# Kernel optimization log

Measured on AMD Instinct MI355X. Metric: run time of the kernel, lower is better.

The kernel has to match this reference:

```python
import jax, jax.numpy as jnp
import numpy as np

B, CI, HI, WI = 64, 3, 96, 96
G = 8
HG, WG = 16, 16
HIDLIN = 512
SIGMA_BOOST = 2.0
EPS = 1e-7
HID = (HI // 4 // 2) * (WI // 4 // 2) * 128  # 12*12*128 = 18432


def _conv(x, w, b):
    # NCHW conv, 3x3, padding 1 (matches nn.Conv2d(kernel_size=3, padding=1))
    y = jax.lax.conv_general_dilated(x, w, (1, 1), ((1, 1), (1, 1)),
                                     dimension_numbers=('NCHW', 'OIHW', 'NCHW'))
    return y + b[None, :, None, None]


def _maxpool(x, k):
    return jax.lax.reduce_window(x, -jnp.inf, jax.lax.max,
                                 (1, 1, k, k), (1, 1, k, k), 'VALID')


def setup_inputs() -> dict:
    key = jax.random.key(0)
    ks = jax.random.split(key, 22)

    def w(k, shape, fan_in):
        return jax.random.normal(k, shape, jnp.float32) * np.float32(1.0 / np.sqrt(fan_in))

    return {
        'image': jax.random.normal(ks[0], (B, CI, HI, WI), jnp.float32),
        'noise': jax.random.normal(ks[1], (B * G, 2), jnp.float32),
        # conv block 1
        'w1a': w(ks[2], (32, CI, 3, 3), CI * 9), 'b1a': jnp.zeros((32,), jnp.float32),
        'w1b': w(ks[3], (32, 32, 3, 3), 32 * 9), 'b1b': jnp.zeros((32,), jnp.float32),
        # conv block 2
        'w2a': w(ks[4], (64, 32, 3, 3), 32 * 9), 'b2a': jnp.zeros((64,), jnp.float32),
        'w2b': w(ks[5], (64, 64, 3, 3), 64 * 9), 'b2b': jnp.zeros((64,), jnp.float32),
        # conv block 3
        'w3a': w(ks[6], (128, 64, 3, 3), 64 * 9), 'b3a': jnp.zeros((128,), jnp.float32),
        'w3b': w(ks[7], (128, 128, 3, 3), 128 * 9), 'b3b': jnp.zeros((128,), jnp.float32),
        # linear head (weights stored (in, out))
        'wl1': w(ks[8], (HID, HIDLIN), HID), 'bl1': jnp.zeros((HIDLIN,), jnp.float32),
        'wl2': w(ks[9], (HIDLIN, HIDLIN), HIDLIN), 'bl2': jnp.zeros((HIDLIN,), jnp.float32),
        'wl3': w(ks[10], (HIDLIN, G * 3), HIDLIN), 'bl3': jnp.zeros((G * 3,), jnp.float32),
    }


def reference(image, noise, w1a, b1a, w1b, b1b, w2a, b2a, w2b, b2b,
              w3a, b3a, w3b, b3b, wl1, bl1, wl2, bl2, wl3, bl3):
    # --- preprocess CNN ---
    x = jax.nn.relu(_conv(image, w1a, b1a))
    x = jax.nn.relu(_conv(x, w1b, b1b))
    x = _maxpool(x, 4)
    x = jax.nn.relu(_conv(x, w2a, b2a))
    x = jax.nn.relu(_conv(x, w2b, b2b))
    x = _maxpool(x, 2)
    x = jax.nn.relu(_conv(x, w3a, b3a))
    x = jax.nn.relu(_conv(x, w3b, b3b))
    x = x.reshape(B, -1)                      # Flatten (C,H,W order, like torch .view)
    x = jax.nn.relu(x @ wl1 + bl1)
    x = jax.nn.relu(x @ wl2 + bl2)            # Linear(HIDLIN,HIDLIN) then the extra ReLU
    prep = (x @ wl3 + bl3).reshape(B * G, 3)  # (b*g, 3)

    means = prep[:, :2]                        # (b*g, 2) raw means
    sraw = prep[:, 2]
    # sparse.transform_sigmas: softplus(s + SIGMA_BOOST) + eps, scaled per spatial dim
    sig = jax.nn.softplus(sraw + SIGMA_BOOST) + EPS
    sigmas = sig[:, None] * jnp.array([HI - 1, WI - 1], jnp.float32)  # (b*g, 2)

    # Normal(means, sigmas).sample() -> reparameterized but detached (torch .sample())
    sample = jax.lax.stop_gradient(means + sigmas * noise)
    # sparse.transform_means over size (hi-hg, wi-wg): sigmoid * (size-1), then round
    msize = jnp.array([HI - HG - 1, WI - WG - 1], jnp.float32)
    pts = jnp.round(jax.nn.sigmoid(sample) * msize).astype(jnp.int32).reshape(B, G, 2)

    # glimpse extraction: the original's b*g python slicing loop -> vmapped dynamic_slice
    src = jax.lax.stop_gradient(image)  # original slices image.data (no grad)

    def ext_one(img, p):
        return jax.lax.dynamic_slice(img, (jnp.int32(0), p[0], p[1]), (CI, HG, WG))

    result = jax.vmap(lambda img, ps: jax.vmap(lambda p: ext_one(img, p))(ps))(src, pts)
    # result: (B, G, CI, HG, WG)
    return result, means.reshape(B, G, 2), sigmas.reshape(B, G, 2)
```

## Files before the change

kernel.cpp:

```cpp
#include <hip/hip_runtime.h>
#include <math.h>

constexpr int BB  = 64;
constexpr int CIc = 3;
constexpr int HIc = 96, WIc = 96;
constexpr int Gc  = 8, HGc = 16, WGc = 16;
constexpr int HIDc = 18432;
constexpr int HIDLINc = 512;

using short8 = __attribute__((ext_vector_type(8))) short;
using s4     = __attribute__((ext_vector_type(4))) short;
using f32x16 = __attribute__((ext_vector_type(16))) float;

__device__ inline unsigned short bfr(float f) {
    unsigned int u = __float_as_uint(f);
    u = (u + 0x7FFFu + ((u >> 16) & 1u)) >> 16;
    return (unsigned short)u;
}
__device__ inline float ubf(unsigned short s) {
    return __uint_as_float(((unsigned int)s) << 16);
}

__device__ __attribute__((aligned(16))) unsigned short g_wh[9216];
__device__ __attribute__((aligned(16))) unsigned short g_wm[9216];
__device__ __attribute__((aligned(16))) unsigned short g_wl[9216];

__device__ __attribute__((aligned(16))) unsigned short g_wph[276480];
__device__ __attribute__((aligned(16))) unsigned short g_wpm[276480];
__device__ __attribute__((aligned(16))) unsigned short g_wpl[276480];

__device__ inline void packN_one(const float* __restrict__ w, int CIN, int ofs,
                                 int idx)
{
    int chsz = 288 * CIN;
    int chunk = idx / chsz;
    int t = idx - chunk * chsz;
    int s = t >> 9;
    int rr = t & 511;
    int g = rr >> 8, oc32 = (rr >> 3) & 31, j = rr & 7;
    int nc16 = CIN / 16;
    int tap = s / nc16, c16 = s % nc16;
    int ci = c16 * 16 + g * 8 + j;
    int oc = chunk * 32 + oc32;
    float v = w[((size_t)oc * CIN + ci) * 9 + tap];
    unsigned short h = bfr(v);
    float r1 = v - ubf(h);
    unsigned short m = bfr(r1);
    g_wph[ofs + idx] = h; g_wpm[ofs + idx] = m; g_wpl[ofs + idx] = bfr(r1 - ubf(m));
}

__global__ void pack_all(const float* __restrict__ w1b, const float* __restrict__ w2a,
                         const float* __restrict__ w2b, const float* __restrict__ w3a,
                         const float* __restrict__ w3b)
{
    int idx = blockIdx.x * 256 + threadIdx.x;
    if (idx < 9216) {
        int j = idx & 7, oc = (idx >> 3) & 31, g = (idx >> 8) & 1, s = idx >> 9;
        int ci = 16 * (s & 1) + 8 * g + j;
        int tap = s >> 1;
        float v = w1b[(oc * 32 + ci) * 9 + tap];
        unsigned short h = bfr(v);
        float r1 = v - ubf(h);
        unsigned short m = bfr(r1);
        g_wh[idx] = h; g_wm[idx] = m; g_wl[idx] = bfr(r1 - ubf(m));
    } else if (idx < 27648) {
        packN_one(w2a, 32, 0, idx - 9216);
    } else if (idx < 64512) {
        packN_one(w2b, 64, 18432, idx - 27648);
    } else if (idx < 138240) {
        packN_one(w3a, 64, 55296, idx - 64512);
    } else if (idx < 285696) {
        packN_one(w3b, 128, 129024, idx - 138240);
    }
}

__device__ inline void bz_one(unsigned short* __restrict__ Xh,
                              unsigned short* __restrict__ Xm,
                              unsigned short* __restrict__ Xl,
                              int PAD, int C, int idx)
{
    int RING = 4 * PAD - 4;
    int ci = idx % C;
    int cell = (idx / C) % RING;
    int b = idx / (C * RING);
    int y, x;
    if (cell < PAD)          { y = 0;       x = cell; }
    else if (cell < 2 * PAD) { y = PAD - 1; x = cell - PAD; }
    else { int t = cell - 2 * PAD; y = 1 + (t >> 1); x = (t & 1) ? PAD - 1 : 0; }
    size_t a = ((size_t)(b * PAD + y) * PAD + x) * C + ci;
    Xh[a] = 0; Xm[a] = 0; Xl[a] = 0;
}

__global__ void border_all(unsigned short* X2h, unsigned short* X2m, unsigned short* X2l,
                           unsigned short* X3h, unsigned short* X3m, unsigned short* X3l,
                           unsigned short* X4h, unsigned short* X4m, unsigned short* X4l,
                           unsigned short* X5h, unsigned short* X5m, unsigned short* X5l)
{
    int idx = blockIdx.x * 256 + threadIdx.x;
    if (idx < 204800)        bz_one(X2h, X2m, X2l, 26, 32, idx);
    else if (idx < 614400)   bz_one(X3h, X3m, X3l, 26, 64, idx - 204800);
    else if (idx < 827392)   bz_one(X4h, X4m, X4l, 14, 64, idx - 614400);
    else if (idx < 1253376)  bz_one(X5h, X5m, X5l, 14, 128, idx - 827392);
}

__global__ __launch_bounds__(256)
void conv1ab(const float* __restrict__ image, const float* __restrict__ w1a,
             const float* __restrict__ b1a, const float* __restrict__ b1b,
             unsigned short* __restrict__ X2h, unsigned short* __restrict__ X2m,
             unsigned short* __restrict__ X2l)
{
    const int id    = blockIdx.x;
    const int xcd   = id & 7;
    const int local = id >> 3;
    const int gblk  = xcd * 576 + local;
    const int b  = gblk / 72;
    const int r  = gblk % 72;
    const int yq = r / 3;
    const int xt = r % 3;

    const int tid = threadIdx.x;
    const int wave = tid >> 6, lane = tid & 63;
    const int col = lane & 31, g = lane >> 5;

    __shared__ float s_img[3][8][36];
    __shared__ __align__(16) short s_hml[3][6][34][36];
    __shared__ float s_pool[4][8][2][16];
    __shared__ float s_b1b[32];
    if (tid < 32) s_b1b[tid] = b1b[tid];

    for (int idx = tid; idx < 3 * 8 * 36; idx += 256) {
        int ci = idx / 288;
        int rem = idx - ci * 288;
        int rr = rem / 36, cc = rem - rr * 36;
        int gy = 4 * yq - 2 + rr, gx = 32 * xt - 2 + cc;
        float v = 0.0f;
        if (gy >= 0 && gy < 96 && gx >= 0 && gx < 96)
            v = image[((size_t)(b * 3 + ci) * 96 + gy) * 96 + gx];
        s_img[ci][rr][cc] = v;
    }
    __syncthreads();

    if (tid < 204) {
        int lr = tid / 34, lc = tid - (tid / 34) * 34;
        int gr = 4 * yq - 1 + lr, gc = 32 * xt - 1 + lc;
        bool valid = (gr >= 0 && gr < 96 && gc >= 0 && gc < 96);
        float acc[32];
#pragma unroll
        for (int oc = 0; oc < 32; ++oc) acc[oc] = 0.0f;
        if (valid) {
#pragma unroll
            for (int ci = 0; ci < 3; ++ci) {
                float v[3][3];
#pragma unroll
                for (int dy = 0; dy < 3; ++dy)
#pragma unroll
                    for (int dx = 0; dx < 3; ++dx)
                        v[dy][dx] = s_img[ci][lr + dy][lc + dx];
#pragma unroll
                for (int oc = 0; oc < 32; ++oc) {
                    const float* w9 = w1a + ((size_t)oc * 3 + ci) * 9;
                    float a = acc[oc];
#pragma unroll
                    for (int dy = 0; dy < 3; ++dy)
#pragma unroll
                        for (int dx = 0; dx < 3; ++dx)
                            a = fmaf(v[dy][dx], w9[dy * 3 + dx], a);
                    acc[oc] = a;
                }
            }
        }
#pragma unroll
        for (int q = 0; q < 8; ++q) {
            s4 H, M, L;
#pragma unroll
            for (int i = 0; i < 4; ++i) {
                int oc = q * 4 + i;
                float v = valid ? fmaxf(acc[oc] + b1a[oc], 0.0f) : 0.0f;
                unsigned short h = bfr(v);
                float r1 = v - ubf(h);
                unsigned short m = bfr(r1);
                H[i] = (short)h; M[i] = (short)m; L[i] = (short)bfr(r1 - ubf(m));
            }
            *(s4*)(&s_hml[0][lr][lc][q * 4]) = H;
            *(s4*)(&s_hml[1][lr][lc][q * 4]) = M;
            *(s4*)(&s_hml[2][lr][lc][q * 4]) = L;
        }
    }
    __syncthreads();

    f32x16 acc0 = {0,0,0,0,0,0,0,0,0,0,0,0,0,0,0,0};
    f32x16 acc1 = {0,0,0,0,0,0,0,0,0,0,0,0,0,0,0,0};

#pragma unroll
    for (int s = 0; s < 18; ++s) {
        const int tap = s >> 1;
        const int dy = tap / 3, dx = tap % 3;
        const int half = s & 1;
        const int aidx = s * 512 + g * 256 + col * 8;
        const int coff = half * 16 + g * 8;

        s4 a0 = *(const s4*)(&s_hml[0][wave + dy][col + dx][coff]);
        s4 a1 = *(const s4*)(&s_hml[0][wave + dy][col + dx][coff + 4]);
        s4 b0 = *(const s4*)(&s_hml[1][wave + dy][col + dx][coff]);
        s4 b1 = *(const s4*)(&s_hml[1][wave + dy][col + dx][coff + 4]);
        s4 c0 = *(const s4*)(&s_hml[2][wave + dy][col + dx][coff]);
        s4 c1 = *(const s4*)(&s_hml[2][wave + dy][col + dx][coff + 4]);

        short8 bh = __builtin_shufflevector(a0, a1, 0, 1, 2, 3, 4, 5, 6, 7);
        short8 bm = __builtin_shufflevector(b0, b1, 0, 1, 2, 3, 4, 5, 6, 7);
        short8 bl = __builtin_shufflevector(c0, c1, 0, 1, 2, 3, 4, 5, 6, 7);

        short8 ah = *(const short8*)(g_wh + aidx);
        short8 am = *(const short8*)(g_wm + aidx);
        short8 al = *(const short8*)(g_wl + aidx);

        acc0 = __builtin_amdgcn_mfma_f32_32x32x16_bf16(ah, bh, acc0, 0, 0, 0);
        acc1 = __builtin_amdgcn_mfma_f32_32x32x16_bf16(ah, bm, acc1, 0, 0, 0);
        acc0 = __builtin_amdgcn_mfma_f32_32x32x16_bf16(am, bh, acc0, 0, 0, 0);
        acc1 = __builtin_amdgcn_mfma_f32_32x32x16_bf16(am, bm, acc1, 0, 0, 0);
        acc0 = __builtin_amdgcn_mfma_f32_32x32x16_bf16(al, bh, acc0, 0, 0, 0);
        acc1 = __builtin_amdgcn_mfma_f32_32x32x16_bf16(ah, bl, acc1, 0, 0, 0);
    }

#pragma unroll
    for (int rr = 0; rr < 16; ++rr) {
        int ocr = (rr & 3) + 8 * (rr >> 2) + 4 * g;
        float v = fmaxf(acc0[rr] + acc1[rr] + s_b1b[ocr], 0.0f);
        v = fmaxf(v, __shfl_xor(v, 1));
        v = fmaxf(v, __shfl_xor(v, 2));
        if ((col & 3) == 0) s_pool[wave][col >> 2][g][rr] = v;
    }
    __syncthreads();

    {
        int oc = tid & 31, pc = tid >> 5;
        if (pc < 8) {
            int gg = (oc >> 2) & 1;
            int rr = (oc & 3) + (((oc >> 3) & 3) << 2);
            float mv = s_pool[0][pc][gg][rr];
            mv = fmaxf(mv, s_pool[1][pc][gg][rr]);
            mv = fmaxf(mv, s_pool[2][pc][gg][rr]);
            mv = fmaxf(mv, s_pool[3][pc][gg][rr]);
            unsigned short h = bfr(mv);
            float r1 = mv - ubf(h);
            unsigned short m = bfr(r1);
            size_t oa = ((size_t)(b * 26 + yq + 1) * 26 + xt * 8 + pc + 1) * 32 + oc;
            X2h[oa] = h; X2m[oa] = m; X2l[oa] = bfr(r1 - ubf(m));
        }
    }
}

template<int CIN, int HW, int NCHUNK, int OUTMODE>
__global__ __launch_bounds__(256)
void convN_mfma(const unsigned short* __restrict__ Xh,
                const unsigned short* __restrict__ Xm,
                const unsigned short* __restrict__ Xl,
                int wofs, const float* __restrict__ bias,
                unsigned short* __restrict__ Yh,
                unsigned short* __restrict__ Ym,
                unsigned short* __restrict__ Yl,
                float* __restrict__ Yf)
{
    constexpr int PAD = HW + 2;
    constexpr int NC16 = CIN / 16;
    constexpr int CHSZ = 288 * CIN;
    constexpr int COUT = NCHUNK * 32;

    const int tid = threadIdx.x;
    const int cpx = gridDim.x >> 3;
    const int blk = (blockIdx.x & 7) * cpx + (blockIdx.x >> 3);
    const int wid = blk * 4 + (tid >> 6);
    const int lane = tid & 63;
    const int col = lane & 31, g = lane >> 5;

    const int chunk = wid % NCHUNK;
    const int wt = wid / NCHUNK;
    const int P = wt * 32 + col;
    const int b = P / (HW * HW);
    const int rem = P - b * (HW * HW);
    const int y = rem / HW, x = rem - y * HW;

    const size_t ib = ((size_t)(b * PAD + y) * PAD + x) * CIN + g * 8;
    const int wbase = wofs + chunk * CHSZ;

    f32x16 acc0 = {0,0,0,0,0,0,0,0,0,0,0,0,0,0,0,0};
    f32x16 acc1 = {0,0,0,0,0,0,0,0,0,0,0,0,0,0,0,0};

#pragma unroll
    for (int tap = 0; tap < 9; ++tap) {
        const int dy = tap / 3, dx = tap % 3;
        for (int c16 = 0; c16 < NC16; ++c16) {
            const int s = tap * NC16 + c16;
            const int aidx = wbase + s * 512 + g * 256 + col * 8;
            const size_t xo = ib + (size_t)((dy * PAD + dx) * CIN + c16 * 16);
            short8 ah = *(const short8*)(g_wph + aidx);
            short8 am = *(const short8*)(g_wpm + aidx);
            short8 al = *(const short8*)(g_wpl + aidx);
            short8 bh = *(const short8*)(Xh + xo);
            short8 bm = *(const short8*)(Xm + xo);
            short8 bl = *(const short8*)(Xl + xo);
            acc0 = __builtin_amdgcn_mfma_f32_32x32x16_bf16(ah, bh, acc0, 0, 0, 0);
            acc1 = __builtin_amdgcn_mfma_f32_32x32x16_bf16(ah, bm, acc1, 0, 0, 0);
            acc0 = __builtin_amdgcn_mfma_f32_32x32x16_bf16(am, bh, acc0, 0, 0, 0);
            acc1 = __builtin_amdgcn_mfma_f32_32x32x16_bf16(am, bm, acc1, 0, 0, 0);
            acc0 = __builtin_amdgcn_mfma_f32_32x32x16_bf16(al, bh, acc0, 0, 0, 0);
            acc1 = __builtin_amdgcn_mfma_f32_32x32x16_bf16(ah, bl, acc1, 0, 0, 0);
        }
    }

    if constexpr (OUTMODE == 0) {
        const size_t obase =
            ((size_t)(b * PAD + y + 1) * PAD + (x + 1)) * COUT + chunk * 32;
#pragma unroll
        for (int q = 0; q < 4; ++q) {
            s4 H, M, L;
#pragma unroll
            for (int i = 0; i < 4; ++i) {
                int r = q * 4 + i;
                int ocr = i + 8 * q + 4 * g;
                float v = fmaxf(acc0[r] + acc1[r] + bias[chunk * 32 + ocr], 0.0f);
                unsigned short h = bfr(v);
                float r1 = v - ubf(h);
                unsigned short m = bfr(r1);
                H[i] = (short)h; M[i] = (short)m; L[i] = (short)bfr(r1 - ubf(m));
            }
            *(s4*)(Yh + obase + 8 * q + 4 * g) = H;
            *(s4*)(Ym + obase + 8 * q + 4 * g) = M;
            *(s4*)(Yl + obase + 8 * q + 4 * g) = L;
        }
    } else {
#pragma unroll
        for (int r = 0; r < 16; ++r) {
            int ocr = chunk * 32 + (r & 3) + 8 * (r >> 2) + 4 * g;
            float v = fmaxf(acc0[r] + acc1[r] + bias[ocr], 0.0f);
            Yf[((size_t)(b * COUT + ocr) * HW + y) * HW + x] = v;
        }
    }
}

__global__ __launch_bounds__(256)
void pool2_pack(const float* __restrict__ t2,
                unsigned short* __restrict__ X4h,
                unsigned short* __restrict__ X4m,
                unsigned short* __restrict__ X4l)
{
    int idx = blockIdx.x * 256 + threadIdx.x;
    constexpr int TOT = BB * 144 * 64;
    if (idx >= TOT) return;
    int oc = idx & 63;
    int p = (idx >> 6) % 144;
    int b = idx / (144 * 64);
    int y = p / 12, x = p % 12;
    const float* src = t2 + ((size_t)(b * 64 + oc) * 24 + 2 * y) * 24 + 2 * x;
    float v = fmaxf(fmaxf(src[0], src[1]), fmaxf(src[24], src[25]));
    unsigned short h = bfr(v);
    float r1 = v - ubf(h);
    unsigned short m = bfr(r1);
    size_t oa = ((size_t)(b * 14 + y + 1) * 14 + x + 1) * 64 + oc;
    X4h[oa] = h; X4m[oa] = m; X4l[oa] = bfr(r1 - ubf(m));
}

constexpr int KSPLIT = 64;
__global__ __launch_bounds__(256)
void lin1_partial(const float* __restrict__ x, const float* __restrict__ w,
                  float* __restrict__ partial)
{
    const int j  = threadIdx.x % 64;
    const int bg = threadIdx.x / 64;
    const int jBase = blockIdx.x * 64;
    const int k  = blockIdx.y;
    const int i0 = k * 288;

    __shared__ float s_x[32][64];

    float acc[16];
#pragma unroll
    for (int u = 0; u < 16; ++u) acc[u] = 0.0f;

    for (int ib = 0; ib < 288; ib += 32) {
        __syncthreads();
        {
            int lb = threadIdx.x / 4;
            int lo = (threadIdx.x % 4) * 8;
            const float* src = x + (size_t)lb * HIDc + i0 + ib + lo;
            float4 a0 = *(const float4*)(src);
            float4 a1 = *(const float4*)(src + 4);
            float tmp[8] = {a0.x, a0.y, a0.z, a0.w, a1.x, a1.y, a1.z, a1.w};
#pragma unroll
            for (int r = 0; r < 8; ++r) s_x[lo + r][lb] = tmp[r];
        }
        __syncthreads();

        for (int ii = 0; ii < 32; ++ii) {
            float wv = w[(size_t)(i0 + ib + ii) * HIDLINc + jBase + j];
            const float4* xp = (const float4*)&s_x[ii][bg * 16];
            float4 x0 = xp[0], x1 = xp[1], x2 = xp[2], x3 = xp[3];
            acc[0]  = fmaf(x0.x, wv, acc[0]);
            acc[1]  = fmaf(x0.y, wv, acc[1]);
            acc[2]  = fmaf(x0.z, wv, acc[2]);
            acc[3]  = fmaf(x0.w, wv, acc[3]);
            acc[4]  = fmaf(x1.x, wv, acc[4]);
            acc[5]  = fmaf(x1.y, wv, acc[5]);
            acc[6]  = fmaf(x1.z, wv, acc[6]);
            acc[7]  = fmaf(x1.w, wv, acc[7]);
            acc[8]  = fmaf(x2.x, wv, acc[8]);
            acc[9]  = fmaf(x2.y, wv, acc[9]);
            acc[10] = fmaf(x2.z, wv, acc[10]);
            acc[11] = fmaf(x2.w, wv, acc[11]);
            acc[12] = fmaf(x3.x, wv, acc[12]);
            acc[13] = fmaf(x3.y, wv, acc[13]);
            acc[14] = fmaf(x3.z, wv, acc[14]);
            acc[15] = fmaf(x3.w, wv, acc[15]);
        }
    }

#pragma unroll
    for (int u = 0; u < 16; ++u) {
        int b = bg * 16 + u;
        partial[((size_t)k * 64 + b) * HIDLINc + jBase + j] = acc[u];
    }
}

__global__ void lin1_reduce(const float* __restrict__ partial,
                            const float* __restrict__ bias,
                            float* __restrict__ x1)
{
    int idx = blockIdx.x * blockDim.x + threadIdx.x;
    if (idx >= 64 * HIDLINc) return;
    int j = idx % HIDLINc;
    float s = 0.0f;
    for (int k = 0; k < KSPLIT; ++k)
        s += partial[(size_t)k * 64 * HIDLINc + idx];
    x1[idx] = fmaxf(s + bias[j], 0.0f);
}

__global__ __launch_bounds__(256)
void lin2_k(const float* __restrict__ x1, const float* __restrict__ w,
            const float* __restrict__ bias, float* __restrict__ x2)
{
    const int j  = threadIdx.x % 64;
    const int bl = threadIdx.x / 64;
    const int jBase = blockIdx.x * 64;
    const int b = blockIdx.y * 4 + bl;

    __shared__ float s_x[4][HIDLINc];
    for (int idx = threadIdx.x; idx < 4 * HIDLINc; idx += 256)
        s_x[idx / HIDLINc][idx % HIDLINc] =
            x1[(size_t)(blockIdx.y * 4 + idx / HIDLINc) * HIDLINc + idx % HIDLINc];
    __syncthreads();

    float acc = 0.0f;
    for (int i = 0; i < HIDLINc; ++i)
        acc = fmaf(s_x[bl][i], w[(size_t)i * HIDLINc + jBase + j], acc);
    x2[(size_t)b * HIDLINc + jBase + j] = fmaxf(acc + bias[jBase + j], 0.0f);
}

__global__ void lin3_k(const float* __restrict__ x2, const float* __restrict__ w,
                       const float* __restrict__ bias, float* __restrict__ prep)
{
    int idx = blockIdx.x * blockDim.x + threadIdx.x;
    if (idx >= 64 * 24) return;
    int j = idx % 24, b = idx / 24;
    float acc = bias[j];
    for (int i = 0; i < HIDLINc; ++i)
        acc = fmaf(x2[(size_t)b * HIDLINc + i], w[i * 24 + j], acc);
    prep[idx] = acc;
}

__global__ void head_k(const float* __restrict__ prep, const float* __restrict__ noise,
                       float* __restrict__ outMeans, float* __restrict__ outSigmas,
                       int* __restrict__ pts)
{
    int id = blockIdx.x * blockDim.x + threadIdx.x;
    if (id >= BB * Gc) return;
    float m0 = prep[id * 3 + 0];
    float m1 = prep[id * 3 + 1];
    float sraw = prep[id * 3 + 2];
    float s = sraw + 2.0f;
    float sig = fmaxf(s, 0.0f) + log1pf(expf(-fabsf(s)));
    sig += 1e-7f;
    float sg = sig * 95.0f;
    outMeans[id * 2 + 0] = m0;
    outMeans[id * 2 + 1] = m1;
    outSigmas[id * 2 + 0] = sg;
    outSigmas[id * 2 + 1] = sg;
    float sa0 = m0 + sg * noise[id * 2 + 0];
    float sa1 = m1 + sg * noise[id * 2 + 1];
    float t0 = 1.0f / (1.0f + expf(-sa0));
    float t1 = 1.0f / (1.0f + expf(-sa1));
    pts[id * 2 + 0] = (int)rintf(t0 * 79.0f);
    pts[id * 2 + 1] = (int)rintf(t1 * 79.0f);
}

__global__ __launch_bounds__(256)
void patch_k(const float* __restrict__ image, const int* __restrict__ pts,
             float* __restrict__ outR)
{
    int id = blockIdx.x;
    int b = id / Gc;
    int p0 = pts[id * 2 + 0];
    int p1 = pts[id * 2 + 1];
    for (int idx = threadIdx.x; idx < CIc * HGc * WGc; idx += 256) {
        int c = idx / (HGc * WGc), rem = idx % (HGc * WGc);
        int hh = rem / WGc, ww = rem % WGc;
        outR[(size_t)id * (CIc * HGc * WGc) + idx] =
            image[((size_t)(b * CIc + c) * HIc + p0 + hh) * WIc + p1 + ww];
    }
}

extern "C" void kernel_launch(void* const* d_in, const int* in_sizes, int n_in,
                              void* d_out, int out_size, void* d_ws, size_t ws_size,
                              hipStream_t stream)
{
    const float* image = (const float*)d_in[0];
    const float* noise = (const float*)d_in[1];
    const float* w1a = (const float*)d_in[2];
    const float* b1a = (const float*)d_in[3];
    const float* w1b = (const float*)d_in[4];
    const float* b1b = (const float*)d_in[5];
    const float* w2a = (const float*)d_in[6];
    const float* b2a = (const float*)d_in[7];
    const float* w2b = (const float*)d_in[8];
    const float* b2b = (const float*)d_in[9];
    const float* w3a = (const float*)d_in[10];
    const float* b3a = (const float*)d_in[11];
    const float* w3b = (const float*)d_in[12];
    const float* b3b = (const float*)d_in[13];
    const float* wl1 = (const float*)d_in[14];
    const float* bl1 = (const float*)d_in[15];
    const float* wl2 = (const float*)d_in[16];
    const float* bl2 = (const float*)d_in[17];
    const float* wl3 = (const float*)d_in[18];
    const float* bl3 = (const float*)d_in[19];

    float* out = (float*)d_out;
    float* ws  = (float*)d_ws;

    unsigned short* X2h = (unsigned short*)(ws + 29884416);
    unsigned short* X2m = (unsigned short*)(ws + 30670848);
    unsigned short* X2l = (unsigned short*)(ws + 31457280);
    unsigned short* X3h = (unsigned short*)(ws);
    unsigned short* X3m = (unsigned short*)(ws + 1572864);
    unsigned short* X3l = (unsigned short*)(ws + 3145728);
    float*  t2  = ws + 4718592;
    unsigned short* X4h = (unsigned short*)(ws + 7340032);
    unsigned short* X4m = (unsigned short*)(ws + 7864320);
    unsigned short* X4l = (unsigned short*)(ws + 8388608);
    unsigned short* X5h = (unsigned short*)(ws + 8912896);
    unsigned short* X5m = (unsigned short*)(ws + 11010048);
    unsigned short* X5l = (unsigned short*)(ws + 12058624);
    float*  t5  = ws + 13107200;
    float*  part= ws + 14680064;
    float*  x1  = ws + 16777216;
    float*  x2  = x1 + 32768;
    float*  prep= x2 + 32768;
    int*    pts = (int*)(prep + 2048);

    pack_all<<<1116, 256, 0, stream>>>(w1b, w2a, w2b, w3a, w3b);

    border_all<<<4896, 256, 0, stream>>>(X2h, X2m, X2l, X3h, X3m, X3l,
                                         X4h, X4m, X4l, X5h, X5m, X5l);

    conv1ab<<<4608, 256, 0, stream>>>(image, w1a, b1a, b1b, X2h, X2m, X2l);

    convN_mfma<32, 24, 2, 0><<<576, 256, 0, stream>>>(
        X2h, X2m, X2l, 0, b2a, X3h, X3m, X3l, nullptr);
    convN_mfma<64, 24, 2, 1><<<576, 256, 0, stream>>>(
        X3h, X3m, X3l, 18432, b2b, nullptr, nullptr, nullptr, t2);
    pool2_pack<<<2304, 256, 0, stream>>>(t2, X4h, X4m, X4l);
    convN_mfma<64, 12, 4, 0><<<288, 256, 0, stream>>>(
        X4h, X4m, X4l, 55296, b3a, X5h, X5m, X5l, nullptr);
    convN_mfma<128, 12, 4, 1><<<288, 256, 0, stream>>>(
        X5h, X5m, X5l, 129024, b3b, nullptr, nullptr, nullptr, t5);

    lin1_partial<<<dim3(8, KSPLIT), 256, 0, stream>>>(t5, wl1, part);
    lin1_reduce<<<(64 * HIDLINc + 255) / 256, 256, 0, stream>>>(part, bl1, x1);
    lin2_k<<<dim3(8, 16), 256, 0, stream>>>(x1, wl2, bl2, x2);
    lin3_k<<<6, 256, 0, stream>>>(x2, wl3, bl3, prep);
    head_k<<<2, 256, 0, stream>>>(prep, noise,
                                  out + (size_t)BB * Gc * CIc * HGc * WGc,
                                  out + (size_t)BB * Gc * CIc * HGc * WGc + BB * Gc * 2,
                                  pts);
    patch_k<<<BB * Gc, 256, 0, stream>>>(image, pts, out);
}
```

Before: 388.3 us.

## Split conv1ab channel staging into halves and alias shared buffers for occupancy

The fused conv1a+conv1b kernel now computes and stages the 32 conv1a output channels in two halves of 16, which roughly halves the hi/mid/lo bf16 staging buffer. The image tile and the pooling scratch now share one aliased shared-memory region, and the launch bounds ask for 5 blocks per CU. The goal is lower LDS and register use per block so more blocks fit on a CU. The cost is an extra block-wide barrier and a second pass of the scalar conv1a loop, plus possible register spills under the tighter bound.

Result: no change. 392.7 us (+1.1%).

```diff
diff --git a/kernel.cpp b/kernel.cpp
--- a/kernel.cpp
+++ b/kernel.cpp
@@ -103,7 +103,7 @@
     else if (idx < 1253376)  bz_one(X5h, X5m, X5l, 14, 128, idx - 827392);
 }
 
-__global__ __launch_bounds__(256)
+__global__ __launch_bounds__(256, 5)
 void conv1ab(const float* __restrict__ image, const float* __restrict__ w1a,
              const float* __restrict__ b1a, const float* __restrict__ b1b,
              unsigned short* __restrict__ X2h, unsigned short* __restrict__ X2m,
@@ -122,10 +122,11 @@
     const int wave = tid >> 6, lane = tid & 63;
     const int col = lane & 31, g = lane >> 5;
 
-    __shared__ float s_img[3][8][36];
-    __shared__ __align__(16) short s_hml[3][6][34][36];
-    __shared__ float s_pool[4][8][2][16];
+    __shared__ __align__(16) short s_hml[3][6][34][20];
+    __shared__ __align__(16) char  s_u[4096];
     __shared__ float s_b1b[32];
+    float (*s_img)[8][36]    = (float(*)[8][36])s_u;
+    float (*s_pool)[8][2][16] = (float(*)[8][2][16])s_u;
     if (tid < 32) s_b1b[tid] = b1b[tid];
 
     for (int idx = tid; idx < 3 * 8 * 36; idx += 256) {
@@ -140,87 +141,96 @@
     }
     __syncthreads();
 
-    if (tid < 204) {
-        int lr = tid / 34, lc = tid - (tid / 34) * 34;
-        int gr = 4 * yq - 1 + lr, gc = 32 * xt - 1 + lc;
-        bool valid = (gr >= 0 && gr < 96 && gc >= 0 && gc < 96);
-        float acc[32];
-#pragma unroll
-        for (int oc = 0; oc < 32; ++oc) acc[oc] = 0.0f;
-        if (valid) {
-#pragma unroll
-            for (int ci = 0; ci < 3; ++ci) {
-                float v[3][3];
-#pragma unroll
-                for (int dy = 0; dy < 3; ++dy)
-#pragma unroll
-                    for (int dx = 0; dx < 3; ++dx)
-                        v[dy][dx] = s_img[ci][lr + dy][lc + dx];
-#pragma unroll
-                for (int oc = 0; oc < 32; ++oc) {
-                    const float* w9 = w1a + ((size_t)oc * 3 + ci) * 9;
-                    float a = acc[oc];
+    const int lr = (tid < 204) ? tid / 34 : 0;
+    const int lc = (tid < 204) ? tid - (tid / 34) * 34 : 0;
+    const int gr = 4 * yq - 1 + lr, gc = 32 * xt - 1 + lc;
+    const bool valid = (tid < 204) && (gr >= 0 && gr < 96 && gc >= 0 && gc < 96);
+
+    f32x16 acc0 = {0,0,0,0,0,0,0,0,0,0,0,0,0,0,0,0};
+    f32x16 acc1 = {0,0,0,0,0,0,0,0,0,0,0,0,0,0,0,0};
+
+#pragma unroll
+    for (int half = 0; half < 2; ++half) {
+        if (half) __syncthreads();
+
+        if (tid < 204) {
+            float acc[16];
+#pragma unroll
+            for (int oc = 0; oc < 16; ++oc) acc[oc] = 0.0f;
+            if (valid) {
+#pragma unroll
+                for (int ci = 0; ci < 3; ++ci) {
+                    float v[3][3];
 #pragma unroll
                     for (int dy = 0; dy < 3; ++dy)
 #pragma unroll
                         for (int dx = 0; dx < 3; ++dx)
-                            a = fmaf(v[dy][dx], w9[dy * 3 + dx], a);
-                    acc[oc] = a;
+                            v[dy][dx] = s_img[ci][lr + dy][lc + dx];
+#pragma unroll
+                    for (int oc = 0; oc < 16; ++oc) {
+                        const float* w9 =
+                            w1a + ((size_t)(half * 16 + oc) * 3 + ci) * 9;
+                        float a = acc[oc];
+#pragma unroll
+                        for (int dy = 0; dy < 3; ++dy)
+#pragma unroll
+                            for (int dx = 0; dx < 3; ++dx)
+                                a = fmaf(v[dy][dx], w9[dy * 3 + dx], a);
+                        acc[oc] = a;
+                    }
                 }
             }
-        }
-#pragma unroll
-        for (int q = 0; q < 8; ++q) {
-            s4 H, M, L;
-#pragma unroll
-            for (int i = 0; i < 4; ++i) {
-                int oc = q * 4 + i;
-                float v = valid ? fmaxf(acc[oc] + b1a[oc], 0.0f) : 0.0f;
-                unsigned short h = bfr(v);
-                float r1 = v - ubf(h);
-                unsigned short m = bfr(r1);
-                H[i] = (short)h; M[i] = (short)m; L[i] = (short)bfr(r1 - ubf(m));
+#pragma unroll
+            for (int q = 0; q < 4; ++q) {
+                s4 H, M, L;
+#pragma unroll
+                for (int i = 0; i < 4; ++i) {
+                    int oc = q * 4 + i;
+                    float v = valid ?
+                        fmaxf(acc[oc] + b1a[half * 16 + oc], 0.0f) : 0.0f;
+                    unsigned short h = bfr(v);
+                    float r1 = v - ubf(h);
+                    unsigned short m = bfr(r1);
+                    H[i] = (short)h; M[i] = (short)m;
+                    L[i] = (short)bfr(r1 - ubf(m));
+                }
+                *(s4*)(&s_hml[0][lr][lc][q * 4]) = H;
+                *(s4*)(&s_hml[1][lr][lc][q * 4]) = M;
+                *(s4*)(&s_hml[2][lr][lc][q * 4]) = L;
             }
-            *(s4*)(&s_hml[0][lr][lc][q * 4]) = H;
-            *(s4*)(&s_hml[1][lr][lc][q * 4]) = M;
-            *(s4*)(&s_hml[2][lr][lc][q * 4]) = L;
+        }
+        __syncthreads();
+
+#pragma unroll
+        for (int tap = 0; tap < 9; ++tap) {
+            const int s = tap * 2 + half;
+            const int dy = tap / 3, dx = tap % 3;
+            const int aidx = s * 512 + g * 256 + col * 8;
+
+            s4 a0 = *(const s4*)(&s_hml[0][wave + dy][col + dx][g * 8]);
+            s4 a1 = *(const s4*)(&s_hml[0][wave + dy][col + dx][g * 8 + 4]);
+            s4 b0 = *(const s4*)(&s_hml[1][wave + dy][col + dx][g * 8]);
+            s4 b1 = *(const s4*)(&s_hml[1][wave + dy][col + dx][g * 8 + 4]);
+            s4 c0 = *(const s4*)(&s_hml[2][wave + dy][col + dx][g * 8]);
+            s4 c1 = *(const s4*)(&s_hml[2][wave + dy][col + dx][g * 8 + 4]);
+
+            short8 bh = __builtin_shufflevector(a0, a1, 0, 1, 2, 3, 4, 5, 6, 7);
+            short8 bm = __builtin_shufflevector(b0, b1, 0, 1, 2, 3, 4, 5, 6, 7);
+            short8 bl = __builtin_shufflevector(c0, c1, 0, 1, 2, 3, 4, 5, 6, 7);
+
+            short8 ah = *(const short8*)(g_wh + aidx);
+            short8 am = *(const short8*)(g_wm + aidx);
+            short8 al = *(const short8*)(g_wl + aidx);
+
+            acc0 = __builtin_amdgcn_mfma_f32_32x32x16_bf16(ah, bh, acc0, 0, 0, 0);
+            acc1 = __builtin_amdgcn_mfma_f32_32x32x16_bf16(ah, bm, acc1, 0, 0, 0);
+            acc0 = __builtin_amdgcn_mfma_f32_32x32x16_bf16(am, bh, acc0, 0, 0, 0);
+            acc1 = __builtin_amdgcn_mfma_f32_32x32x16_bf16(am, bm, acc1, 0, 0, 0);
+            acc0 = __builtin_amdgcn_mfma_f32_32x32x16_bf16(al, bh, acc0, 0, 0, 0);
+            acc1 = __builtin_amdgcn_mfma_f32_32x32x16_bf16(ah, bl, acc1, 0, 0, 0);
         }
     }
     __syncthreads();
-
-    f32x16 acc0 = {0,0,0,0,0,0,0,0,0,0,0,0,0,0,0,0};
-    f32x16 acc1 = {0,0,0,0,0,0,0,0,0,0,0,0,0,0,0,0};
-
-#pragma unroll
-    for (int s = 0; s < 18; ++s) {
-        const int tap = s >> 1;
-        const int dy = tap / 3, dx = tap % 3;
-        const int half = s & 1;
-        const int aidx = s * 512 + g * 256 + col * 8;
-        const int coff = half * 16 + g * 8;
-
-        s4 a0 = *(const s4*)(&s_hml[0][wave + dy][col + dx][coff]);
-        s4 a1 = *(const s4*)(&s_hml[0][wave + dy][col + dx][coff + 4]);
-        s4 b0 = *(const s4*)(&s_hml[1][wave + dy][col + dx][coff]);
-        s4 b1 = *(const s4*)(&s_hml[1][wave + dy][col + dx][coff + 4]);
-        s4 c0 = *(const s4*)(&s_hml[2][wave + dy][col + dx][coff]);
-        s4 c1 = *(const s4*)(&s_hml[2][wave + dy][col + dx][coff + 4]);
-
-        short8 bh = __builtin_shufflevector(a0, a1, 0, 1, 2, 3, 4, 5, 6, 7);
-        short8 bm = __builtin_shufflevector(b0, b1, 0, 1, 2, 3, 4, 5, 6, 7);
-        short8 bl = __builtin_shufflevector(c0, c1, 0, 1, 2, 3, 4, 5, 6, 7);
-
-        short8 ah = *(const short8*)(g_wh + aidx);
-        short8 am = *(const short8*)(g_wm + aidx);
-        short8 al = *(const short8*)(g_wl + aidx);
-
-        acc0 = __builtin_amdgcn_mfma_f32_32x32x16_bf16(ah, bh, acc0, 0, 0, 0);
-        acc1 = __builtin_amdgcn_mfma_f32_32x32x16_bf16(ah, bm, acc1, 0, 0, 0);
-        acc0 = __builtin_amdgcn_mfma_f32_32x32x16_bf16(am, bh, acc0, 0, 0, 0);
-        acc1 = __builtin_amdgcn_mfma_f32_32x32x16_bf16(am, bm, acc1, 0, 0, 0);
-        acc0 = __builtin_amdgcn_mfma_f32_32x32x16_bf16(al, bh, acc0, 0, 0, 0);
-        acc1 = __builtin_amdgcn_mfma_f32_32x32x16_bf16(ah, bl, acc1, 0, 0, 0);
-    }
 
 #pragma unroll
     for (int rr = 0; rr < 16; ++rr) {
```
